# Optimization experiments

Measured on AMD Instinct MI355X. Metric: run time of the kernel, lower is better.

## Reference

```python
import jax, jax.numpy as jnp
import numpy as np

NUM_GRAPHS = 512  # number of segments (graphs) in the batch


def setup_inputs() -> dict:
    key = jax.random.key(0)
    k1, k2, k3, k4, k5, k6 = jax.random.split(key, 6)
    N, Din, D, H = 100000, 1024, 64, 32
    x = jax.random.normal(k1, (N, Din), dtype=jnp.float32)
    batch = jnp.sort(jax.random.randint(k2, (N,), 0, NUM_GRAPHS)).astype(jnp.int64)
    W_enc = jax.random.normal(k3, (D, Din), dtype=jnp.float32) * (1.0 / np.sqrt(Din))
    b_enc = jax.random.normal(k4, (D,), dtype=jnp.float32) * 0.01
    W_gate = jax.random.normal(k5, (H, D), dtype=jnp.float32) * (1.0 / np.sqrt(D))
    b_gate = jax.random.normal(k6, (H,), dtype=jnp.float32) * 0.01
    return {"x": x, "batch": batch, "W_enc": W_enc, "b_enc": b_enc,
            "W_gate": W_gate, "b_gate": b_gate}


def reference(x, batch, W_enc, b_enc, W_gate, b_gate):
    B = NUM_GRAPHS
    batch = batch.astype(jnp.int32)
    # shared encoder: [N, Din] -> [N, D]
    xe = jnp.dot(x, W_enc.T) + b_enc
    # all 32 heads' scalar gates at once: [N, H]
    gate = jnp.dot(xe, W_gate.T) + b_gate
    # segment-wise (per-graph) stable softmax over nodes, per head
    gmax = jax.ops.segment_max(gate, batch, num_segments=B)          # [B, H]
    g = jnp.exp(gate - gmax[batch])                                   # [N, H]
    gsum = jax.ops.segment_sum(g, batch, num_segments=B)             # [B, H]
    alpha = g / gsum[batch]                                           # [N, H]
    # scatter-weighted sum: out[b,h,d] = sum_{n in graph b} alpha[n,h]*xe[n,d]
    weighted = alpha[:, :, None] * xe[:, None, :]                     # [N, H, D]
    pooled = jax.ops.segment_sum(weighted, batch, num_segments=B)    # [B, H, D]
    # concat over heads (head i occupies cols [i*D, (i+1)*D)) then ReLU
    return jax.nn.relu(pooled.reshape(B, -1))
```

## Files before the change

kernel.cpp:

```cpp
#include <hip/hip_runtime.h>


typedef short bf16x8 __attribute__((ext_vector_type(8)));
typedef float f32x4 __attribute__((ext_vector_type(4)));

#define NUM_GRAPHS 512
#define DIN 1024
#define DENC 64
#define NH 32
#define NB 96
#define BK 32
#define LDA 40
#define LDB 40

__device__ __forceinline__ unsigned short f2bf(float f) {
    unsigned int u = __float_as_uint(f);
    return (unsigned short)((u + 0x7fffu + ((u >> 16) & 1u)) >> 16);
}
__device__ __forceinline__ void split2(float f, unsigned short& h, unsigned short& l) {
    unsigned int u = __float_as_uint(f);
    unsigned int hb = (u + 0x7fffu + ((u >> 16) & 1u)) >> 16;
    h = (unsigned short)hb;
    float hf = __uint_as_float(hb << 16);
    l = f2bf(f - hf);
}

__device__ __forceinline__ int clampseg(int v) {
    return v < 0 ? 0 : (v >= NUM_GRAPHS ? NUM_GRAPHS - 1 : v);
}

__global__ void k_prep(const int* __restrict__ batch, int* __restrict__ seg, int N,
                       const float* __restrict__ W,
                       const float* __restrict__ Wg,
                       const float* __restrict__ bg,
                       const float* __restrict__ be,
                       unsigned short* __restrict__ Wh,
                       unsigned short* __restrict__ Wl,
                       float* __restrict__ bcomb,
                       int nseg_blocks, int nconv_blocks)
{
    const int blk = blockIdx.x;
    const int tid = threadIdx.x;
    if (blk < nseg_blocks) {
        int n = blk * 256 + tid;
        if (n >= N) return;
        int bc = clampseg(batch[n]);
        if (n == 0) {
            for (int j = 0; j <= bc; ++j) seg[j] = 0;
            int bl = clampseg(batch[N - 1]);
            for (int j = bl + 1; j <= NUM_GRAPHS; ++j) seg[j] = N;
        } else {
            int bp = clampseg(batch[n - 1]);
            for (int j = bp + 1; j <= bc; ++j) seg[j] = n;
        }
    } else if (blk < nseg_blocks + nconv_blocks) {
        int idx = ((blk - nseg_blocks) * 256 + tid) * 4;
        float4 v = *(const float4*)(W + idx);
        ushort4 h4, l4;
        split2(v.x, h4.x, l4.x);
        split2(v.y, h4.y, l4.y);
        split2(v.z, h4.z, l4.z);
        split2(v.w, h4.w, l4.w);
        *(ushort4*)(Wh + idx) = h4;
        *(ushort4*)(Wl + idx) = l4;
    } else {
        __shared__ float wgr[DENC];
        const int j = blk - nseg_blocks - nconv_blocks;
        if (tid < DENC) wgr[tid] = Wg[j * DENC + tid];
        __syncthreads();
        const int k0 = tid * 4;
        float4 a = {0.f, 0.f, 0.f, 0.f};
        for (int d = 0; d < DENC; ++d) {
            float w = wgr[d];
            float4 v = *(const float4*)(W + d * DIN + k0);
            a.x += w * v.x; a.y += w * v.y; a.z += w * v.z; a.w += w * v.w;
        }
        ushort4 h4, l4;
        split2(a.x, h4.x, l4.x);
        split2(a.y, h4.y, l4.y);
        split2(a.z, h4.z, l4.z);
        split2(a.w, h4.w, l4.w);
        *(ushort4*)(Wh + (DENC + j) * DIN + k0) = h4;
        *(ushort4*)(Wl + (DENC + j) * DIN + k0) = l4;
        if (tid == 0) {
            float s = bg[j];
            for (int d = 0; d < DENC; ++d) s += wgr[d] * be[d];
            bcomb[j] = s;
        }
    }
}

__global__ __launch_bounds__(256, 4) void k_gemm(
    const float* __restrict__ x,
    const unsigned short* __restrict__ Wh,
    const unsigned short* __restrict__ Wl,
    const float* __restrict__ b_enc,
    const float* __restrict__ bcomb,
    float* __restrict__ xe,
    float* __restrict__ gate,
    int N)
{
    __shared__ unsigned short Ah[128 * LDA], Al[128 * LDA];
    __shared__ unsigned short Bh[NB * LDB],  Bl[NB * LDB];

    const int tid  = threadIdx.x;
    const int lane = tid & 63;
    const int wv   = tid >> 6;
    const long brow = (long)blockIdx.x * 128;

    f32x4 acc[2][6];
    #pragma unroll
    for (int i = 0; i < 2; ++i)
        #pragma unroll
        for (int j = 0; j < 6; ++j) acc[i][j] = (f32x4){0.f, 0.f, 0.f, 0.f};

    const int arow = tid >> 1;
    const int ac16 = (tid & 1) * 16;
    const int fr  = lane & 15;
    const int fq  = lane >> 4;

    float4  va[4];
    ushort4 vbh[3], vbl[3];

    const long arowg = brow + arow;
    const bool arok = (arowg < N);
    const float* aptr = x + arowg * DIN + ac16;

    auto loadA = [&](int kc) {
        #pragma unroll
        for (int i = 0; i < 4; ++i)
            va[i] = arok ? *(const float4*)(aptr + kc + 4 * i)
                         : (float4){0.f, 0.f, 0.f, 0.f};
    };
    auto loadB = [&](int kc) {
        #pragma unroll
        for (int i = 0; i < 3; ++i) {
            int idx = tid + 256 * i;
            int row = idx >> 3;
            int c4  = (idx & 7) * 4;
            vbh[i] = *(const ushort4*)(Wh + row * DIN + kc + c4);
            vbl[i] = *(const ushort4*)(Wl + row * DIN + kc + c4);
        }
    };
    auto stageA = [&]() {
        #pragma unroll
        for (int i = 0; i < 4; ++i) {
            ushort4 h4, l4;
            split2(va[i].x, h4.x, l4.x);
            split2(va[i].y, h4.y, l4.y);
            split2(va[i].z, h4.z, l4.z);
            split2(va[i].w, h4.w, l4.w);
            *(ushort4*)&Ah[arow * LDA + ac16 + 4 * i] = h4;
            *(ushort4*)&Al[arow * LDA + ac16 + 4 * i] = l4;
        }
    };
    auto stageB = [&]() {
        #pragma unroll
        for (int i = 0; i < 3; ++i) {
            int idx = tid + 256 * i;
            int row = idx >> 3;
            int c4  = (idx & 7) * 4;
            *(ushort4*)&Bh[row * LDB + c4] = vbh[i];
            *(ushort4*)&Bl[row * LDB + c4] = vbl[i];
        }
    };
    auto mfmaPhase = [&]() {
        bf16x8 ah[2], al[2];
        #pragma unroll
        for (int rt = 0; rt < 2; ++rt) {
            int o = (wv * 32 + rt * 16 + fr) * LDA + fq * 8;
            ah[rt] = *(const bf16x8*)&Ah[o];
            al[rt] = *(const bf16x8*)&Al[o];
        }
        #pragma unroll
        for (int ct = 0; ct < 6; ++ct) {
            int o = (ct * 16 + fr) * LDB + fq * 8;
            bf16x8 bh = *(const bf16x8*)&Bh[o];
            bf16x8 bl = *(const bf16x8*)&Bl[o];
            #pragma unroll
            for (int rt = 0; rt < 2; ++rt) {
                acc[rt][ct] = __builtin_amdgcn_mfma_f32_16x16x32_bf16(ah[rt], bh, acc[rt][ct], 0, 0, 0);
                acc[rt][ct] = __builtin_amdgcn_mfma_f32_16x16x32_bf16(ah[rt], bl, acc[rt][ct], 0, 0, 0);
                acc[rt][ct] = __builtin_amdgcn_mfma_f32_16x16x32_bf16(al[rt], bh, acc[rt][ct], 0, 0, 0);
            }
        }
    };

    loadA(0);
    loadB(0);

    for (int k0 = 0; k0 < DIN; k0 += BK) {
        stageA();
        stageB();
        __syncthreads();
        const int kn = k0 + BK;
        if (kn < DIN) {
            loadA(kn);
            loadB(kn);
        }
        mfmaPhase();
        __syncthreads();
    }

    float bv[4], bcv[2];
    #pragma unroll
    for (int ct = 0; ct < 4; ++ct) bv[ct] = b_enc[ct * 16 + fr];
    #pragma unroll
    for (int j = 0; j < 2; ++j) bcv[j] = bcomb[j * 16 + fr];
    #pragma unroll
    for (int rt = 0; rt < 2; ++rt) {
        #pragma unroll
        for (int r = 0; r < 4; ++r) {
            long row = brow + wv * 32 + rt * 16 + fq * 4 + r;
            if (row < N) {
                float* o = xe + row * DENC;
                #pragma unroll
                for (int ct = 0; ct < 4; ++ct)
                    o[ct * 16 + fr] = acc[rt][ct][r] + bv[ct];
                float* g = gate + row * NH;
                #pragma unroll
                for (int j = 0; j < 2; ++j)
                    g[j * 16 + fr] = acc[rt][4 + j][r] + bcv[j];
            }
        }
    }
}

__global__ __launch_bounds__(256) void k_pool(
    const float* __restrict__ xe,
    const float* __restrict__ gate,
    const int* __restrict__ seg,
    float* __restrict__ out,
    int N)
{
    __shared__ float xs[64 * 68];
    __shared__ float gs[64 * 36];
    const int tid = threadIdx.x;
    const int b = blockIdx.x;
    const int s = seg[b], e = seg[b + 1];
    const long ob = (long)b * (NH * DENC);
    if (e <= s) {
        for (int i = tid; i < NH * DENC; i += 256) out[ob + i] = 0.f;
        return;
    }
    const int rl = tid & 63;
    const int hq = tid >> 6;
    const int h0 = hq * 8;
    const int r0s = tid >> 4, c4 = (tid & 15) * 4;

    float m[8], pool[8], gp[8];
    #pragma unroll
    for (int j = 0; j < 8; ++j) { m[j] = -INFINITY; pool[j] = 0.f; gp[j] = 0.f; }

    float4 xv[4];
    float gv[8];
    auto load_chunk = [&](int base, int nrow) {
        #pragma unroll
        for (int i = 0; i < 4; ++i) {
            int row = r0s + 16 * i;
            xv[i] = (row < nrow)
                  ? *(const float4*)(xe + (long)(base + row) * DENC + c4)
                  : (float4){0.f, 0.f, 0.f, 0.f};
        }
        if (rl < nrow) {
            const float* g0 = gate + (long)(base + rl) * NH + h0;
            float4 a = *(const float4*)g0;
            float4 c = *(const float4*)(g0 + 4);
            gv[0] = a.x; gv[1] = a.y; gv[2] = a.z; gv[3] = a.w;
            gv[4] = c.x; gv[5] = c.y; gv[6] = c.z; gv[7] = c.w;
        } else {
            #pragma unroll
            for (int j = 0; j < 8; ++j) gv[j] = -INFINITY;
        }
    };

    load_chunk(s, min(64, e - s));

    for (int base = s; base < e; base += 64) {
        const int nrow = min(64, e - base);
        float cm[8];
        #pragma unroll
        for (int j = 0; j < 8; ++j) cm[j] = gv[j];
        #pragma unroll
        for (int off = 32; off > 0; off >>= 1)
            #pragma unroll
            for (int j = 0; j < 8; ++j) cm[j] = fmaxf(cm[j], __shfl_xor(cm[j], off));
        #pragma unroll
        for (int j = 0; j < 8; ++j) {
            if (cm[j] > m[j]) {
                float sc = (m[j] == -INFINITY) ? 0.f : __expf(m[j] - cm[j]);
                pool[j] *= sc;
                gp[j]   *= sc;
                m[j] = cm[j];
            }
        }
        float4 ga, gb;
        ga.x = __expf(gv[0] - m[0]); ga.y = __expf(gv[1] - m[1]);
        ga.z = __expf(gv[2] - m[2]); ga.w = __expf(gv[3] - m[3]);
        gb.x = __expf(gv[4] - m[4]); gb.y = __expf(gv[5] - m[5]);
        gb.z = __expf(gv[6] - m[6]); gb.w = __expf(gv[7] - m[7]);
        gp[0] += ga.x; gp[1] += ga.y; gp[2] += ga.z; gp[3] += ga.w;
        gp[4] += gb.x; gp[5] += gb.y; gp[6] += gb.z; gp[7] += gb.w;
        #pragma unroll
        for (int i = 0; i < 4; ++i)
            *(float4*)&xs[(r0s + 16 * i) * 68 + c4] = xv[i];
        *(float4*)&gs[rl * 36 + h0] = ga;
        *(float4*)&gs[rl * 36 + h0 + 4] = gb;
        int nb = base + 64;
        if (nb < e) load_chunk(nb, min(64, e - nb));
        __syncthreads();
        #pragma unroll 4
        for (int r2 = 0; r2 < nrow; ++r2) {
            float xvv = xs[r2 * 68 + rl];
            float4 g1 = *(const float4*)&gs[r2 * 36 + h0];
            float4 g2 = *(const float4*)&gs[r2 * 36 + h0 + 4];
            pool[0] += g1.x * xvv; pool[1] += g1.y * xvv;
            pool[2] += g1.z * xvv; pool[3] += g1.w * xvv;
            pool[4] += g2.x * xvv; pool[5] += g2.y * xvv;
            pool[6] += g2.z * xvv; pool[7] += g2.w * xvv;
        }
        __syncthreads();
    }
    #pragma unroll
    for (int off = 32; off > 0; off >>= 1)
        #pragma unroll
        for (int j = 0; j < 8; ++j) gp[j] += __shfl_xor(gp[j], off);
    #pragma unroll
    for (int j = 0; j < 8; ++j) {
        float v = pool[j] / gp[j];
        out[ob + (h0 + j) * DENC + rl] = fmaxf(v, 0.f);
    }
}

extern "C" void kernel_launch(void* const* d_in, const int* in_sizes, int n_in,
                              void* d_out, int out_size, void* d_ws, size_t ws_size,
                              hipStream_t stream)
{
    const float* x      = (const float*)d_in[0];
    const int* batch    = (const int*)d_in[1];
    const float* W_enc  = (const float*)d_in[2];
    const float* b_enc  = (const float*)d_in[3];
    const float* W_gate = (const float*)d_in[4];
    const float* b_gate = (const float*)d_in[5];
    float* out = (float*)d_out;
    const int N = in_sizes[1];

    char* ws = (char*)d_ws;
    size_t off = 0;
    auto take = [&](size_t bytes) {
        char* p = ws + off;
        off += (bytes + 255) & ~(size_t)255;
        return p;
    };
    float* xe   = (float*)take((size_t)N * DENC * sizeof(float));
    float* gate = (float*)take((size_t)N * NH * sizeof(float));
    unsigned short* Wh = (unsigned short*)take((size_t)NB * DIN * 2);
    unsigned short* Wl = (unsigned short*)take((size_t)NB * DIN * 2);
    float* bcomb = (float*)take(NH * sizeof(float));
    int* seg = (int*)take((NUM_GRAPHS + 1) * sizeof(int));
    (void)ws_size; (void)n_in; (void)out_size;

    const int nseg_blocks  = (N + 255) / 256;
    const int nconv_blocks = (DENC * DIN) / 1024;
    k_prep<<<nseg_blocks + nconv_blocks + NH, 256, 0, stream>>>(
        batch, seg, N, W_enc, W_gate, b_gate, b_enc, Wh, Wl, bcomb, nseg_blocks, nconv_blocks);
    k_gemm<<<(N + 127) / 128, 256, 0, stream>>>(x, Wh, Wl, b_enc, bcomb, xe, gate, N);
    k_pool<<<NUM_GRAPHS, 256, 0, stream>>>(xe, gate, seg, out, N);
}
```

Measured before the change: 623.0 us.

## Fuse segment softmax pooling into GEMM epilogue with atomic accumulation

The GEMM epilogue now stages each 128-row tile of xe and exp(gate) in shared memory, which reuses the GEMM buffers through a union. It reduces runs of rows that share a segment and atomically adds the weighted sums and gate sums into per-graph accumulators. A small final kernel divides by the gate sum and applies ReLU. This removes the round trip of the xe and gate intermediates through global memory, along with the segment-offset pass and the per-graph serial pooling kernel. In exchange, it drops the per-segment max subtraction, which risks exp overflow for large gate values, and makes the float summation order nondeterministic because of the atomics.

```diff
diff --git a/kernel.cpp b/kernel.cpp
--- a/kernel.cpp
+++ b/kernel.cpp
@@ -29,32 +29,19 @@
     return v < 0 ? 0 : (v >= NUM_GRAPHS ? NUM_GRAPHS - 1 : v);
 }
 
-__global__ void k_prep(const int* __restrict__ batch, int* __restrict__ seg, int N,
-                       const float* __restrict__ W,
+__global__ void k_prep(const float* __restrict__ W,
                        const float* __restrict__ Wg,
                        const float* __restrict__ bg,
                        const float* __restrict__ be,
                        unsigned short* __restrict__ Wh,
                        unsigned short* __restrict__ Wl,
                        float* __restrict__ bcomb,
-                       int nseg_blocks, int nconv_blocks)
+                       float* __restrict__ accp)
 {
     const int blk = blockIdx.x;
     const int tid = threadIdx.x;
-    if (blk < nseg_blocks) {
-        int n = blk * 256 + tid;
-        if (n >= N) return;
-        int bc = clampseg(batch[n]);
-        if (n == 0) {
-            for (int j = 0; j <= bc; ++j) seg[j] = 0;
-            int bl = clampseg(batch[N - 1]);
-            for (int j = bl + 1; j <= NUM_GRAPHS; ++j) seg[j] = N;
-        } else {
-            int bp = clampseg(batch[n - 1]);
-            for (int j = bp + 1; j <= bc; ++j) seg[j] = n;
-        }
-    } else if (blk < nseg_blocks + nconv_blocks) {
-        int idx = ((blk - nseg_blocks) * 256 + tid) * 4;
+    if (blk < 64) {
+        int idx = (blk * 256 + tid) * 4;
         float4 v = *(const float4*)(W + idx);
         ushort4 h4, l4;
         split2(v.x, h4.x, l4.x);
@@ -63,9 +50,9 @@
         split2(v.w, h4.w, l4.w);
         *(ushort4*)(Wh + idx) = h4;
         *(ushort4*)(Wl + idx) = l4;
-    } else {
+    } else if (blk < 96) {
         __shared__ float wgr[DENC];
-        const int j = blk - nseg_blocks - nconv_blocks;
+        const int j = blk - 64;
         if (tid < DENC) wgr[tid] = Wg[j * DENC + tid];
         __syncthreads();
         const int k0 = tid * 4;
@@ -87,8 +74,17 @@
             for (int d = 0; d < DENC; ++d) s += wgr[d] * be[d];
             bcomb[j] = s;
         }
-    }
-}
+    } else {
+        int idx = ((blk - 96) * 256 + tid) * 4;
+        *(float4*)(accp + idx) = (float4){0.f, 0.f, 0.f, 0.f};
+    }
+}
+
+union SMem {
+    struct { unsigned short Ah[128 * LDA]; unsigned short Al[128 * LDA];
+             unsigned short Bh[NB * LDB];  unsigned short Bl[NB * LDB]; } s;
+    struct { float xs[64 * 68]; float gs[64 * 36]; int sg[128]; } e;
+};
 
 __global__ __launch_bounds__(256, 4) void k_gemm(
     const float* __restrict__ x,
@@ -96,12 +92,12 @@
     const unsigned short* __restrict__ Wl,
     const float* __restrict__ b_enc,
     const float* __restrict__ bcomb,
-    float* __restrict__ xe,
-    float* __restrict__ gate,
+    const int* __restrict__ batch,
+    float* __restrict__ accp,
+    float* __restrict__ accg,
     int N)
 {
-    __shared__ unsigned short Ah[128 * LDA], Al[128 * LDA];
-    __shared__ unsigned short Bh[NB * LDB],  Bl[NB * LDB];
+    __shared__ SMem sm;
 
     const int tid  = threadIdx.x;
     const int lane = tid & 63;
@@ -150,8 +146,8 @@
             split2(va[i].y, h4.y, l4.y);
             split2(va[i].z, h4.z, l4.z);
             split2(va[i].w, h4.w, l4.w);
-            *(ushort4*)&Ah[arow * LDA + ac16 + 4 * i] = h4;
-            *(ushort4*)&Al[arow * LDA + ac16 + 4 * i] = l4;
+            *(ushort4*)&sm.s.Ah[arow * LDA + ac16 + 4 * i] = h4;
+            *(ushort4*)&sm.s.Al[arow * LDA + ac16 + 4 * i] = l4;
         }
     };
     auto stageB = [&]() {
@@ -160,8 +156,8 @@
             int idx = tid + 256 * i;
             int row = idx >> 3;
             int c4  = (idx & 7) * 4;
-            *(ushort4*)&Bh[row * LDB + c4] = vbh[i];
-            *(ushort4*)&Bl[row * LDB + c4] = vbl[i];
+            *(ushort4*)&sm.s.Bh[row * LDB + c4] = vbh[i];
+            *(ushort4*)&sm.s.Bl[row * LDB + c4] = vbl[i];
         }
     };
     auto mfmaPhase = [&]() {
@@ -169,14 +165,14 @@
         #pragma unroll
         for (int rt = 0; rt < 2; ++rt) {
             int o = (wv * 32 + rt * 16 + fr) * LDA + fq * 8;
-            ah[rt] = *(const bf16x8*)&Ah[o];
-            al[rt] = *(const bf16x8*)&Al[o];
+            ah[rt] = *(const bf16x8*)&sm.s.Ah[o];
+            al[rt] = *(const bf16x8*)&sm.s.Al[o];
         }
         #pragma unroll
         for (int ct = 0; ct < 6; ++ct) {
             int o = (ct * 16 + fr) * LDB + fq * 8;
-            bf16x8 bh = *(const bf16x8*)&Bh[o];
-            bf16x8 bl = *(const bf16x8*)&Bl[o];
+            bf16x8 bh = *(const bf16x8*)&sm.s.Bh[o];
+            bf16x8 bl = *(const bf16x8*)&sm.s.Bl[o];
             #pragma unroll
             for (int rt = 0; rt < 2; ++rt) {
                 acc[rt][ct] = __builtin_amdgcn_mfma_f32_16x16x32_bf16(ah[rt], bh, acc[rt][ct], 0, 0, 0);
@@ -207,128 +203,93 @@
     for (int ct = 0; ct < 4; ++ct) bv[ct] = b_enc[ct * 16 + fr];
     #pragma unroll
     for (int j = 0; j < 2; ++j) bcv[j] = bcomb[j * 16 + fr];
-    #pragma unroll
-    for (int rt = 0; rt < 2; ++rt) {
-        #pragma unroll
-        for (int r = 0; r < 4; ++r) {
-            long row = brow + wv * 32 + rt * 16 + fq * 4 + r;
-            if (row < N) {
-                float* o = xe + row * DENC;
+
+    if (tid < 128) {
+        long gr = brow + tid;
+        int  ix = (int)((gr < N) ? gr : (N - 1));
+        sm.e.sg[tid] = clampseg(batch[ix]);
+    }
+
+    const int h0 = wv * 8;
+    const int rl = lane;
+    float pool[8], gp[8];
+
+    auto flush = [&](int sgid) {
+        if (gp[0] != 0.f) {
+            float* pp = accp + ((long)sgid * NH + h0) * DENC + rl;
+            #pragma unroll
+            for (int j = 0; j < 8; ++j) {
+                atomicAdd(pp + j * DENC, pool[j]);
+                pool[j] = 0.f;
+            }
+            if (rl == 0) {
                 #pragma unroll
-                for (int ct = 0; ct < 4; ++ct)
-                    o[ct * 16 + fr] = acc[rt][ct][r] + bv[ct];
-                float* g = gate + row * NH;
+                for (int j = 0; j < 8; ++j) {
+                    atomicAdd(accg + sgid * NH + h0 + j, gp[j]);
+                }
+            }
+        }
+        #pragma unroll
+        for (int j = 0; j < 8; ++j) gp[j] = 0.f;
+    };
+
+    #pragma unroll
+    for (int half = 0; half < 2; ++half) {
+        if ((wv >> 1) == half) {
+            #pragma unroll
+            for (int rt = 0; rt < 2; ++rt) {
                 #pragma unroll
-                for (int j = 0; j < 2; ++j)
-                    g[j * 16 + fr] = acc[rt][4 + j][r] + bcv[j];
+                for (int r = 0; r < 4; ++r) {
+                    int  lr = (wv & 1) * 32 + rt * 16 + fq * 4 + r;
+                    long gr = brow + half * 64 + lr;
+                    bool ok = (gr < N);
+                    #pragma unroll
+                    for (int ct = 0; ct < 4; ++ct)
+                        sm.e.xs[lr * 68 + ct * 16 + fr] = acc[rt][ct][r] + bv[ct];
+                    #pragma unroll
+                    for (int j = 0; j < 2; ++j)
+                        sm.e.gs[lr * 36 + j * 16 + fr] =
+                            ok ? __expf(acc[rt][4 + j][r] + bcv[j]) : 0.f;
+                }
             }
         }
-    }
-}
-
-__global__ __launch_bounds__(256) void k_pool(
-    const float* __restrict__ xe,
-    const float* __restrict__ gate,
-    const int* __restrict__ seg,
-    float* __restrict__ out,
-    int N)
+        __syncthreads();
+
+        #pragma unroll
+        for (int j = 0; j < 8; ++j) { pool[j] = 0.f; gp[j] = 0.f; }
+        int cur = sm.e.sg[half * 64];
+        for (int r2 = 0; r2 < 64; ++r2) {
+            int s2 = sm.e.sg[half * 64 + r2];
+            if (s2 != cur) { flush(cur); cur = s2; }
+            float  xv = sm.e.xs[r2 * 68 + rl];
+            float4 g1 = *(const float4*)&sm.e.gs[r2 * 36 + h0];
+            float4 g2 = *(const float4*)&sm.e.gs[r2 * 36 + h0 + 4];
+            pool[0] += g1.x * xv; pool[1] += g1.y * xv;
+            pool[2] += g1.z * xv; pool[3] += g1.w * xv;
+            pool[4] += g2.x * xv; pool[5] += g2.y * xv;
+            pool[6] += g2.z * xv; pool[7] += g2.w * xv;
+            gp[0] += g1.x; gp[1] += g1.y; gp[2] += g1.z; gp[3] += g1.w;
+            gp[4] += g2.x; gp[5] += g2.y; gp[6] += g2.z; gp[7] += g2.w;
+        }
+        flush(cur);
+        __syncthreads();
+    }
+}
+
+__global__ __launch_bounds__(256) void k_final(
+    const float* __restrict__ accp,
+    const float* __restrict__ accg,
+    float* __restrict__ out)
 {
-    __shared__ float xs[64 * 68];
-    __shared__ float gs[64 * 36];
-    const int tid = threadIdx.x;
     const int b = blockIdx.x;
-    const int s = seg[b], e = seg[b + 1];
-    const long ob = (long)b * (NH * DENC);
-    if (e <= s) {
-        for (int i = tid; i < NH * DENC; i += 256) out[ob + i] = 0.f;
-        return;
-    }
-    const int rl = tid & 63;
-    const int hq = tid >> 6;
-    const int h0 = hq * 8;
-    const int r0s = tid >> 4, c4 = (tid & 15) * 4;
-
-    float m[8], pool[8], gp[8];
-    #pragma unroll
-    for (int j = 0; j < 8; ++j) { m[j] = -INFINITY; pool[j] = 0.f; gp[j] = 0.f; }
-
-    float4 xv[4];
-    float gv[8];
-    auto load_chunk = [&](int base, int nrow) {
-        #pragma unroll
-        for (int i = 0; i < 4; ++i) {
-            int row = r0s + 16 * i;
-            xv[i] = (row < nrow)
-                  ? *(const float4*)(xe + (long)(base + row) * DENC + c4)
-                  : (float4){0.f, 0.f, 0.f, 0.f};
-        }
-        if (rl < nrow) {
-            const float* g0 = gate + (long)(base + rl) * NH + h0;
-            float4 a = *(const float4*)g0;
-            float4 c = *(const float4*)(g0 + 4);
-            gv[0] = a.x; gv[1] = a.y; gv[2] = a.z; gv[3] = a.w;
-            gv[4] = c.x; gv[5] = c.y; gv[6] = c.z; gv[7] = c.w;
-        } else {
-            #pragma unroll
-            for (int j = 0; j < 8; ++j) gv[j] = -INFINITY;
-        }
-    };
-
-    load_chunk(s, min(64, e - s));
-
-    for (int base = s; base < e; base += 64) {
-        const int nrow = min(64, e - base);
-        float cm[8];
-        #pragma unroll
-        for (int j = 0; j < 8; ++j) cm[j] = gv[j];
-        #pragma unroll
-        for (int off = 32; off > 0; off >>= 1)
-            #pragma unroll
-            for (int j = 0; j < 8; ++j) cm[j] = fmaxf(cm[j], __shfl_xor(cm[j], off));
-        #pragma unroll
-        for (int j = 0; j < 8; ++j) {
-            if (cm[j] > m[j]) {
-                float sc = (m[j] == -INFINITY) ? 0.f : __expf(m[j] - cm[j]);
-                pool[j] *= sc;
-                gp[j]   *= sc;
-                m[j] = cm[j];
-            }
-        }
-        float4 ga, gb;
-        ga.x = __expf(gv[0] - m[0]); ga.y = __expf(gv[1] - m[1]);
-        ga.z = __expf(gv[2] - m[2]); ga.w = __expf(gv[3] - m[3]);
-        gb.x = __expf(gv[4] - m[4]); gb.y = __expf(gv[5] - m[5]);
-        gb.z = __expf(gv[6] - m[6]); gb.w = __expf(gv[7] - m[7]);
-        gp[0] += ga.x; gp[1] += ga.y; gp[2] += ga.z; gp[3] += ga.w;
-        gp[4] += gb.x; gp[5] += gb.y; gp[6] += gb.z; gp[7] += gb.w;
-        #pragma unroll
-        for (int i = 0; i < 4; ++i)
-            *(float4*)&xs[(r0s + 16 * i) * 68 + c4] = xv[i];
-        *(float4*)&gs[rl * 36 + h0] = ga;
-        *(float4*)&gs[rl * 36 + h0 + 4] = gb;
-        int nb = base + 64;
-        if (nb < e) load_chunk(nb, min(64, e - nb));
-        __syncthreads();
-        #pragma unroll 4
-        for (int r2 = 0; r2 < nrow; ++r2) {
-            float xvv = xs[r2 * 68 + rl];
-            float4 g1 = *(const float4*)&gs[r2 * 36 + h0];
-            float4 g2 = *(const float4*)&gs[r2 * 36 + h0 + 4];
-            pool[0] += g1.x * xvv; pool[1] += g1.y * xvv;
-            pool[2] += g1.z * xvv; pool[3] += g1.w * xvv;
-            pool[4] += g2.x * xvv; pool[5] += g2.y * xvv;
-            pool[6] += g2.z * xvv; pool[7] += g2.w * xvv;
-        }
-        __syncthreads();
-    }
-    #pragma unroll
-    for (int off = 32; off > 0; off >>= 1)
-        #pragma unroll
-        for (int j = 0; j < 8; ++j) gp[j] += __shfl_xor(gp[j], off);
-    #pragma unroll
-    for (int j = 0; j < 8; ++j) {
-        float v = pool[j] / gp[j];
-        out[ob + (h0 + j) * DENC + rl] = fmaxf(v, 0.f);
+    const float* pp = accp + (long)b * (NH * DENC);
+    float* oo = out + (long)b * (NH * DENC);
+    #pragma unroll
+    for (int it = 0; it < 8; ++it) {
+        int i = threadIdx.x + 256 * it;
+        float s = accg[b * NH + (i >> 6)];
+        float v = (s > 0.f) ? pp[i] / s : 0.f;
+        oo[i] = fmaxf(v, 0.f);
     }
 }
 
@@ -352,18 +313,14 @@
         off += (bytes + 255) & ~(size_t)255;
         return p;
     };
-    float* xe   = (float*)take((size_t)N * DENC * sizeof(float));
-    float* gate = (float*)take((size_t)N * NH * sizeof(float));
+    float* accp = (float*)take((size_t)NUM_GRAPHS * NH * DENC * sizeof(float));
+    float* accg = (float*)take((size_t)NUM_GRAPHS * NH * sizeof(float));
     unsigned short* Wh = (unsigned short*)take((size_t)NB * DIN * 2);
     unsigned short* Wl = (unsigned short*)take((size_t)NB * DIN * 2);
     float* bcomb = (float*)take(NH * sizeof(float));
-    int* seg = (int*)take((NUM_GRAPHS + 1) * sizeof(int));
     (void)ws_size; (void)n_in; (void)out_size;
 
-    const int nseg_blocks  = (N + 255) / 256;
-    const int nconv_blocks = (DENC * DIN) / 1024;
-    k_prep<<<nseg_blocks + nconv_blocks + NH, 256, 0, stream>>>(
-        batch, seg, N, W_enc, W_gate, b_gate, b_enc, Wh, Wl, bcomb, nseg_blocks, nconv_blocks);
-    k_gemm<<<(N + 127) / 128, 256, 0, stream>>>(x, Wh, Wl, b_enc, bcomb, xe, gate, N);
-    k_pool<<<NUM_GRAPHS, 256, 0, stream>>>(xe, gate, seg, out, N);
-}
+    k_prep<<<1136, 256, 0, stream>>>(W_enc, W_gate, b_gate, b_enc, Wh, Wl, bcomb, accp);
+    k_gemm<<<(N + 127) / 128, 256, 0, stream>>>(x, Wh, Wl, b_enc, bcomb, batch, accp, accg, N);
+    k_final<<<NUM_GRAPHS, 256, 0, stream>>>(accp, accg, out);
+}
```

Measured after the change: 654.3 us. 5.0% more time.

## Load GEMM A operand straight into MFMA fragment registers, skipping LDS staging

Applied to the files above, without the earlier changes.

The GEMM kernel no longer stages the fp32 x tile through shared memory. Each lane loads its own MFMA fragment directly from global memory and splits it into bf16 hi/lo in registers. The block tile shrinks from 128 to 64 rows (one 16-row tile per wave) and the K step grows from 32 to 64. B is now staged synchronously, without register prefetch. This removes the LDS writes and reads for A, trading them for less coalesced global loads of A, more blocks, and more repeated B traffic per row.

```diff
diff --git a/kernel.cpp b/kernel.cpp
--- a/kernel.cpp
+++ b/kernel.cpp
@@ -9,9 +9,8 @@
 #define DENC 64
 #define NH 32
 #define NB 96
-#define BK 32
-#define LDA 40
-#define LDB 40
+#define BKG 64
+#define LDBG 72
 
 __device__ __forceinline__ unsigned short f2bf(float f) {
     unsigned int u = __float_as_uint(f);
@@ -100,105 +99,81 @@
     float* __restrict__ gate,
     int N)
 {
-    __shared__ unsigned short Ah[128 * LDA], Al[128 * LDA];
-    __shared__ unsigned short Bh[NB * LDB],  Bl[NB * LDB];
+    __shared__ unsigned short Bh[NB * LDBG], Bl[NB * LDBG];
 
     const int tid  = threadIdx.x;
     const int lane = tid & 63;
     const int wv   = tid >> 6;
-    const long brow = (long)blockIdx.x * 128;
-
-    f32x4 acc[2][6];
-    #pragma unroll
-    for (int i = 0; i < 2; ++i)
-        #pragma unroll
-        for (int j = 0; j < 6; ++j) acc[i][j] = (f32x4){0.f, 0.f, 0.f, 0.f};
-
-    const int arow = tid >> 1;
-    const int ac16 = (tid & 1) * 16;
+    const long brow = (long)blockIdx.x * 64;
     const int fr  = lane & 15;
     const int fq  = lane >> 4;
 
-    float4  va[4];
-    ushort4 vbh[3], vbl[3];
-
-    const long arowg = brow + arow;
-    const bool arok = (arowg < N);
-    const float* aptr = x + arowg * DIN + ac16;
-
+    f32x4 acc[6];
+    #pragma unroll
+    for (int j = 0; j < 6; ++j) acc[j] = (f32x4){0.f, 0.f, 0.f, 0.f};
+
+    const long arow = brow + wv * 16 + fr;
+    const bool aok  = (arow < N);
+    const float* ap = x + arow * DIN + fq * 8;
+
+    float4 va[4];
     auto loadA = [&](int kc) {
-        #pragma unroll
-        for (int i = 0; i < 4; ++i)
-            va[i] = arok ? *(const float4*)(aptr + kc + 4 * i)
-                         : (float4){0.f, 0.f, 0.f, 0.f};
+        if (aok) {
+            va[0] = *(const float4*)(ap + kc);
+            va[1] = *(const float4*)(ap + kc + 4);
+            va[2] = *(const float4*)(ap + kc + 32);
+            va[3] = *(const float4*)(ap + kc + 36);
+        } else {
+            #pragma unroll
+            for (int i = 0; i < 4; ++i) va[i] = (float4){0.f, 0.f, 0.f, 0.f};
+        }
     };
-    auto loadB = [&](int kc) {
-        #pragma unroll
-        for (int i = 0; i < 3; ++i) {
-            int idx = tid + 256 * i;
-            int row = idx >> 3;
-            int c4  = (idx & 7) * 4;
-            vbh[i] = *(const ushort4*)(Wh + row * DIN + kc + c4);
-            vbl[i] = *(const ushort4*)(Wl + row * DIN + kc + c4);
+
+    auto stageB = [&](int kc) {
+        #pragma unroll
+        for (int i = 0; i < 6; ++i) {
+            int c   = tid + 256 * i;
+            int row = c >> 4;
+            int c4  = (c & 15) * 4;
+            *(ushort4*)&Bh[row * LDBG + c4] = *(const ushort4*)(Wh + row * DIN + kc + c4);
+            *(ushort4*)&Bl[row * LDBG + c4] = *(const ushort4*)(Wl + row * DIN + kc + c4);
         }
     };
-    auto stageA = [&]() {
-        #pragma unroll
-        for (int i = 0; i < 4; ++i) {
-            ushort4 h4, l4;
-            split2(va[i].x, h4.x, l4.x);
-            split2(va[i].y, h4.y, l4.y);
-            split2(va[i].z, h4.z, l4.z);
-            split2(va[i].w, h4.w, l4.w);
-            *(ushort4*)&Ah[arow * LDA + ac16 + 4 * i] = h4;
-            *(ushort4*)&Al[arow * LDA + ac16 + 4 * i] = l4;
-        }
-    };
-    auto stageB = [&]() {
-        #pragma unroll
-        for (int i = 0; i < 3; ++i) {
-            int idx = tid + 256 * i;
-            int row = idx >> 3;
-            int c4  = (idx & 7) * 4;
-            *(ushort4*)&Bh[row * LDB + c4] = vbh[i];
-            *(ushort4*)&Bl[row * LDB + c4] = vbl[i];
-        }
-    };
-    auto mfmaPhase = [&]() {
+
+    loadA(0);
+
+    for (int k0 = 0; k0 < DIN; k0 += BKG) {
+        stageB(k0);
+        __syncthreads();
+
         bf16x8 ah[2], al[2];
         #pragma unroll
-        for (int rt = 0; rt < 2; ++rt) {
-            int o = (wv * 32 + rt * 16 + fr) * LDA + fq * 8;
-            ah[rt] = *(const bf16x8*)&Ah[o];
-            al[rt] = *(const bf16x8*)&Al[o];
-        }
+        for (int K = 0; K < 2; ++K) {
+            const float f[8] = { va[2*K].x, va[2*K].y, va[2*K].z, va[2*K].w,
+                                 va[2*K+1].x, va[2*K+1].y, va[2*K+1].z, va[2*K+1].w };
+            #pragma unroll
+            for (int e = 0; e < 8; ++e) {
+                unsigned short h, l;
+                split2(f[e], h, l);
+                ah[K][e] = (short)h;
+                al[K][e] = (short)l;
+            }
+        }
+        const int kn = k0 + BKG;
+        if (kn < DIN) loadA(kn);
+
         #pragma unroll
         for (int ct = 0; ct < 6; ++ct) {
-            int o = (ct * 16 + fr) * LDB + fq * 8;
-            bf16x8 bh = *(const bf16x8*)&Bh[o];
-            bf16x8 bl = *(const bf16x8*)&Bl[o];
-            #pragma unroll
-            for (int rt = 0; rt < 2; ++rt) {
-                acc[rt][ct] = __builtin_amdgcn_mfma_f32_16x16x32_bf16(ah[rt], bh, acc[rt][ct], 0, 0, 0);
-                acc[rt][ct] = __builtin_amdgcn_mfma_f32_16x16x32_bf16(ah[rt], bl, acc[rt][ct], 0, 0, 0);
-                acc[rt][ct] = __builtin_amdgcn_mfma_f32_16x16x32_bf16(al[rt], bh, acc[rt][ct], 0, 0, 0);
+            #pragma unroll
+            for (int K = 0; K < 2; ++K) {
+                int o = (ct * 16 + fr) * LDBG + fq * 8 + K * 32;
+                bf16x8 bh = *(const bf16x8*)&Bh[o];
+                bf16x8 bl = *(const bf16x8*)&Bl[o];
+                acc[ct] = __builtin_amdgcn_mfma_f32_16x16x32_bf16(ah[K], bh, acc[ct], 0, 0, 0);
+                acc[ct] = __builtin_amdgcn_mfma_f32_16x16x32_bf16(ah[K], bl, acc[ct], 0, 0, 0);
+                acc[ct] = __builtin_amdgcn_mfma_f32_16x16x32_bf16(al[K], bh, acc[ct], 0, 0, 0);
             }
         }
-    };
-
-    loadA(0);
-    loadB(0);
-
-    for (int k0 = 0; k0 < DIN; k0 += BK) {
-        stageA();
-        stageB();
-        __syncthreads();
-        const int kn = k0 + BK;
-        if (kn < DIN) {
-            loadA(kn);
-            loadB(kn);
-        }
-        mfmaPhase();
         __syncthreads();
     }
 
@@ -208,20 +183,17 @@
     #pragma unroll
     for (int j = 0; j < 2; ++j) bcv[j] = bcomb[j * 16 + fr];
     #pragma unroll
-    for (int rt = 0; rt < 2; ++rt) {
-        #pragma unroll
-        for (int r = 0; r < 4; ++r) {
-            long row = brow + wv * 32 + rt * 16 + fq * 4 + r;
-            if (row < N) {
-                float* o = xe + row * DENC;
-                #pragma unroll
-                for (int ct = 0; ct < 4; ++ct)
-                    o[ct * 16 + fr] = acc[rt][ct][r] + bv[ct];
-                float* g = gate + row * NH;
-                #pragma unroll
-                for (int j = 0; j < 2; ++j)
-                    g[j * 16 + fr] = acc[rt][4 + j][r] + bcv[j];
-            }
+    for (int r = 0; r < 4; ++r) {
+        long row = brow + wv * 16 + fq * 4 + r;
+        if (row < N) {
+            float* o = xe + row * DENC;
+            #pragma unroll
+            for (int ct = 0; ct < 4; ++ct)
+                o[ct * 16 + fr] = acc[ct][r] + bv[ct];
+            float* g = gate + row * NH;
+            #pragma unroll
+            for (int j = 0; j < 2; ++j)
+                g[j * 16 + fr] = acc[4 + j][r] + bcv[j];
         }
     }
 }
@@ -364,6 +336,6 @@
     const int nconv_blocks = (DENC * DIN) / 1024;
     k_prep<<<nseg_blocks + nconv_blocks + NH, 256, 0, stream>>>(
         batch, seg, N, W_enc, W_gate, b_gate, b_enc, Wh, Wl, bcomb, nseg_blocks, nconv_blocks);
-    k_gemm<<<(N + 127) / 128, 256, 0, stream>>>(x, Wh, Wl, b_enc, bcomb, xe, gate, N);
+    k_gemm<<<(N + 63) / 64, 256, 0, stream>>>(x, Wh, Wl, b_enc, bcomb, xe, gate, N);
     k_pool<<<NUM_GRAPHS, 256, 0, stream>>>(xe, gate, seg, out, N);
 }
```

Result: faster. 600.1 us (-3.7%).
